# Kernel tuning notes

Measured on AMD Instinct MI355X. Metric: run time of the kernel, lower is better.

## Reference

```python
import jax, jax.numpy as jnp
import numpy as np

EMBED_DIM = 768
NUM_HEADS = 12


def setup_inputs() -> dict:
    key = jax.random.key(0)
    ks = jax.random.split(key, 9)
    C = EMBED_DIM
    x = jax.random.normal(ks[0], (8, 3136, C), dtype=jnp.float32)
    s = 0.02
    Wq = jax.random.normal(ks[1], (C, C), dtype=jnp.float32) * s
    Wk = jax.random.normal(ks[2], (C, C), dtype=jnp.float32) * s
    Wv = jax.random.normal(ks[3], (C, C), dtype=jnp.float32) * s
    Wo = jax.random.normal(ks[4], (C, C), dtype=jnp.float32) * s
    bq = jax.random.normal(ks[5], (C,), dtype=jnp.float32) * s
    bk = jax.random.normal(ks[6], (C,), dtype=jnp.float32) * s
    bv = jax.random.normal(ks[7], (C,), dtype=jnp.float32) * s
    bo = jax.random.normal(ks[8], (C,), dtype=jnp.float32) * s
    return {"x": x, "Wq": Wq, "bq": bq, "Wk": Wk, "bk": bk,
            "Wv": Wv, "bv": bv, "Wo": Wo, "bo": bo, "T": 16}


def reference(x, Wq, bq, Wk, bk, Wv, bv, Wo, bo, T):
    B, N, C = x.shape
    H = NUM_HEADS
    hd = C // H
    Hh = H // 2
    P = N // T
    scale = 1.0 / np.sqrt(hd).astype(np.float32)

    Q = (x @ Wq + bq).reshape(B, T, P, H, hd)
    K = (x @ Wk + bk).reshape(B, T, P, H, hd)
    V = (x @ Wv + bv).reshape(B, T, P, H, hd)

    # spatial attention: first Hh heads, attend over patches within each frame
    Qs, Ks, Vs = Q[..., :Hh, :], K[..., :Hh, :], V[..., :Hh, :]
    scores_s = jnp.einsum('btphd,btqhd->bthpq', Qs, Ks) * scale  # (B,T,Hh,P,P)
    ws = jax.nn.softmax(scores_s, axis=-1)
    out_s = jnp.einsum('bthpq,btqhd->btphd', ws, Vs)  # (B,T,P,Hh,hd)

    # temporal attention: last Hh heads, attend over frames at each patch
    Qt, Kt, Vt = Q[..., Hh:, :], K[..., Hh:, :], V[..., Hh:, :]
    scores_t = jnp.einsum('btphd,bsphd->bphts', Qt, Kt) * scale  # (B,P,Hh,T,T)
    wt = jax.nn.softmax(scores_t, axis=-1)
    out_t = jnp.einsum('bphts,bsphd->btphd', wt, Vt)  # (B,T,P,Hh,hd)

    out = jnp.concatenate([out_s, out_t], axis=3).reshape(B, N, C)
    return out @ Wo + bo
```

## Files before the change

### kernel.cpp

```cpp
#include <hip/hip_runtime.h>


typedef __attribute__((ext_vector_type(8))) short short8;
typedef __attribute__((ext_vector_type(4))) float f32x4;

typedef __attribute__((address_space(1))) void gvoid;
typedef __attribute__((address_space(3))) void lvoid;

__device__ __forceinline__ unsigned short f2b(float f) {
  unsigned int u = __float_as_uint(f);
  unsigned int r = (u + 0x7FFFu + ((u >> 16) & 1u)) >> 16;
  return (unsigned short)r;
}

__global__ __launch_bounds__(256) void k_convert_x(
    const float* __restrict__ x, unsigned short* __restrict__ xb,
    const float* __restrict__ bq, const float* __restrict__ bk,
    const float* __restrict__ bv, float* __restrict__ bqkv) {
  int tid = blockIdx.x * 256 + threadIdx.x;
  if (tid < 2304)
    bqkv[tid] = tid < 768 ? bq[tid] : (tid < 1536 ? bk[tid - 768] : bv[tid - 1536]);
  float4 v = ((const float4*)x)[tid];
  ushort4 o;
  o.x = f2b(v.x); o.y = f2b(v.y); o.z = f2b(v.z); o.w = f2b(v.w);
  ((ushort4*)xb)[tid] = o;
}

__global__ __launch_bounds__(256) void k_pack_w(
    const float* __restrict__ Wq, const float* __restrict__ Wk,
    const float* __restrict__ Wv, const float* __restrict__ Wo,
    unsigned short* __restrict__ wqkvT, unsigned short* __restrict__ woT) {
  __shared__ float tile[32][33];
  int bid = blockIdx.x;
  const float* W;
  unsigned short* dst;
  int n0, k0;
  if (bid < 1728) {
    int tn = bid % 72, tk = bid / 72;
    n0 = tn * 32; k0 = tk * 32;
    int which = n0 / 768;
    W = which == 0 ? Wq : (which == 1 ? Wk : Wv);
    dst = wqkvT;
  } else {
    int b2 = bid - 1728;
    int tn = b2 % 24, tk = b2 / 24;
    n0 = tn * 32; k0 = tk * 32;
    W = Wo; dst = woT;
  }
  int nn0 = n0 % 768;
  for (int i = threadIdx.x; i < 1024; i += 256) {
    int r = i >> 5, c = i & 31;
    tile[r][c] = W[(size_t)(k0 + r) * 768 + nn0 + c];
  }
  __syncthreads();
  for (int i = threadIdx.x; i < 1024; i += 256) {
    int r = i >> 5, c = i & 31;
    dst[(size_t)(n0 + r) * 768 + k0 + c] = f2b(tile[c][r]);
  }
}

template <int OUTF32>
__global__ __launch_bounds__(256) void k_gemm_bt(
    const unsigned short* __restrict__ A, const unsigned short* __restrict__ Bt,
    const float* __restrict__ bias, void* __restrict__ Cout,
    int M, int N, int K) {
  __shared__ __align__(16) unsigned short As[128 * 32];
  __shared__ __align__(16) unsigned short Bs[128 * 32];
  const int tid = threadIdx.x;
  const int w = tid >> 6, l = tid & 63;
  const int lg = l >> 4, ln = l & 15;
  const int m0 = blockIdx.y * 128, n0 = blockIdx.x * 128;
  const int wr = (w >> 1) * 64, wc = (w & 1) * 64;
  f32x4 acc[4][4] = {};
  const unsigned short* ga = A + (size_t)(m0 + (tid >> 2)) * K + ((tid & 3) * 8);
  const unsigned short* gb = Bt + (size_t)(n0 + (tid >> 2)) * K + ((tid & 3) * 8);
  unsigned short* lAs = As + w * 512;
  unsigned short* lBs = Bs + w * 512;
  const size_t krow64 = (size_t)64 * K;
  for (int k0 = 0; k0 < K; k0 += 32) {
    __builtin_amdgcn_global_load_lds((const gvoid*)(ga + k0),          (lvoid*)lAs,          16, 0, 0);
    __builtin_amdgcn_global_load_lds((const gvoid*)(ga + krow64 + k0), (lvoid*)(lAs + 2048), 16, 0, 0);
    __builtin_amdgcn_global_load_lds((const gvoid*)(gb + k0),          (lvoid*)lBs,          16, 0, 0);
    __builtin_amdgcn_global_load_lds((const gvoid*)(gb + krow64 + k0), (lvoid*)(lBs + 2048), 16, 0, 0);
    __syncthreads();
    short8 a[4], b[4];
#pragma unroll
    for (int mt = 0; mt < 4; ++mt)
      a[mt] = *(const short8*)(As + (wr + mt * 16 + ln) * 32 + lg * 8);
#pragma unroll
    for (int nt = 0; nt < 4; ++nt)
      b[nt] = *(const short8*)(Bs + (wc + nt * 16 + ln) * 32 + lg * 8);
#pragma unroll
    for (int mt = 0; mt < 4; ++mt)
#pragma unroll
      for (int nt = 0; nt < 4; ++nt)
        acc[mt][nt] = __builtin_amdgcn_mfma_f32_16x16x32_bf16(a[mt], b[nt], acc[mt][nt], 0, 0, 0);
    __syncthreads();
  }
#pragma unroll
  for (int nt = 0; nt < 4; ++nt) {
    int col = n0 + wc + nt * 16 + ln;
    float bval = bias[col];
#pragma unroll
    for (int mt = 0; mt < 4; ++mt) {
      int row = m0 + wr + mt * 16 + lg * 4;
#pragma unroll
      for (int r = 0; r < 4; ++r) {
        float v = acc[mt][nt][r] + bval;
        if (OUTF32)
          ((float*)Cout)[(size_t)(row + r) * N + col] = v;
        else
          ((unsigned short*)Cout)[(size_t)(row + r) * N + col] = f2b(v);
      }
    }
  }
}

__global__ __launch_bounds__(256) void k_attn_spatial(
    const unsigned short* __restrict__ qkv, unsigned short* __restrict__ attn) {
  const int bi = blockIdx.x;
  const int h = bi % 6;
  const int t = (bi / 6) % 16;
  const int b = bi / 96;
  const int base_row = b * 3136 + t * 196;
  __shared__ __align__(16) unsigned short Vt[64][232];
  __shared__ __align__(16) unsigned short Pl[4][16][232];
  for (int i = threadIdx.x; i < 196 * 64; i += 256) {
    int key = i >> 6, d = i & 63;
    Vt[d][key] = qkv[(size_t)(base_row + key) * 2304 + 1536 + h * 64 + d];
  }
  for (int i = threadIdx.x; i < 64 * 28; i += 256)
    Vt[i / 28][196 + (i % 28)] = 0;
  __syncthreads();
  const int w = threadIdx.x >> 6, l = threadIdx.x & 63;
  const int lg = l >> 4, ln = l & 15;
  const float scale = 0.125f;
  for (int mt = w; mt < 13; mt += 4) {
    int qm = mt * 16 + ln; if (qm > 195) qm = 195;
    const size_t qoff = (size_t)(base_row + qm) * 2304 + h * 64 + lg * 8;
    short8 qa0 = *(const short8*)(qkv + qoff);
    short8 qa1 = *(const short8*)(qkv + qoff + 32);
    f32x4 st[13];
#pragma unroll
    for (int nt = 0; nt < 13; ++nt) {
      int kn = nt * 16 + ln; if (kn > 195) kn = 195;
      const size_t koff = (size_t)(base_row + kn) * 2304 + 768 + h * 64 + lg * 8;
      short8 kb0 = *(const short8*)(qkv + koff);
      short8 kb1 = *(const short8*)(qkv + koff + 32);
      f32x4 s = {0.f, 0.f, 0.f, 0.f};
      s = __builtin_amdgcn_mfma_f32_16x16x32_bf16(qa0, kb0, s, 0, 0, 0);
      s = __builtin_amdgcn_mfma_f32_16x16x32_bf16(qa1, kb1, s, 0, 0, 0);
      st[nt] = s;
    }
    float mr[4] = {-1e30f, -1e30f, -1e30f, -1e30f};
#pragma unroll
    for (int nt = 0; nt < 13; ++nt) {
      bool valid = (nt * 16 + ln) < 196;
#pragma unroll
      for (int r = 0; r < 4; ++r) {
        float v = valid ? st[nt][r] * scale : -1e30f;
        st[nt][r] = v;
        mr[r] = fmaxf(mr[r], v);
      }
    }
#pragma unroll
    for (int msk = 1; msk <= 8; msk <<= 1)
#pragma unroll
      for (int r = 0; r < 4; ++r) mr[r] = fmaxf(mr[r], __shfl_xor(mr[r], msk));
    float sm[4] = {0.f, 0.f, 0.f, 0.f};
#pragma unroll
    for (int nt = 0; nt < 13; ++nt)
#pragma unroll
      for (int r = 0; r < 4; ++r) {
        float p = __expf(st[nt][r] - mr[r]);
        st[nt][r] = p;
        sm[r] += p;
      }
#pragma unroll
    for (int msk = 1; msk <= 8; msk <<= 1)
#pragma unroll
      for (int r = 0; r < 4; ++r) sm[r] += __shfl_xor(sm[r], msk);
    float inv[4];
#pragma unroll
    for (int r = 0; r < 4; ++r) inv[r] = 1.f / sm[r];
#pragma unroll
    for (int nt = 0; nt < 13; ++nt)
#pragma unroll
      for (int r = 0; r < 4; ++r)
        Pl[w][lg * 4 + r][nt * 16 + ln] = f2b(st[nt][r] * inv[r]);
#pragma unroll
    for (int r = 0; r < 4; ++r) Pl[w][ln][208 + lg * 4 + r] = 0;
#pragma unroll
    for (int nt4 = 0; nt4 < 4; ++nt4) {
      f32x4 acc = {0.f, 0.f, 0.f, 0.f};
#pragma unroll
      for (int ks = 0; ks < 7; ++ks) {
        short8 pa = *(const short8*)(&Pl[w][ln][ks * 32 + lg * 8]);
        short8 vb = *(const short8*)(&Vt[nt4 * 16 + ln][ks * 32 + lg * 8]);
        acc = __builtin_amdgcn_mfma_f32_16x16x32_bf16(pa, vb, acc, 0, 0, 0);
      }
#pragma unroll
      for (int r = 0; r < 4; ++r) {
        int m = mt * 16 + lg * 4 + r;
        if (m < 196)
          attn[(size_t)(base_row + m) * 768 + h * 64 + nt4 * 16 + ln] = f2b(acc[r]);
      }
    }
  }
}

__global__ __launch_bounds__(256) void k_attn_temporal(
    const unsigned short* __restrict__ qkv, unsigned short* __restrict__ attn) {
  const int w = threadIdx.x >> 6, l = threadIdx.x & 63;
  const int u = blockIdx.x * 4 + w;
  const int b = u / 1176;
  const int rem = u % 1176;
  const int p = rem / 6;
  const int h = 6 + rem % 6;
  const size_t rowb = (size_t)b * 3136 + p;
  __shared__ __align__(16) unsigned short Vt[4][64][40];
  __shared__ __align__(16) unsigned short Pl[4][16][40];
  for (int i = l; i < 1024; i += 64) {
    int tt = i >> 6, d = i & 63;
    Vt[w][d][tt] = qkv[(rowb + (size_t)tt * 196) * 2304 + 1536 + h * 64 + d];
  }
  for (int i = l; i < 1024; i += 64)
    Vt[w][i >> 4][16 + (i & 15)] = 0;
  const int lg = l >> 4, ln = l & 15;
  const size_t qoff = (rowb + (size_t)ln * 196) * 2304 + h * 64 + lg * 8;
  short8 qa0 = *(const short8*)(qkv + qoff);
  short8 qa1 = *(const short8*)(qkv + qoff + 32);
  short8 kb0 = *(const short8*)(qkv + qoff + 768);
  short8 kb1 = *(const short8*)(qkv + qoff + 768 + 32);
  f32x4 s = {0.f, 0.f, 0.f, 0.f};
  s = __builtin_amdgcn_mfma_f32_16x16x32_bf16(qa0, kb0, s, 0, 0, 0);
  s = __builtin_amdgcn_mfma_f32_16x16x32_bf16(qa1, kb1, s, 0, 0, 0);
  const float scale = 0.125f;
  float stv[4], mr[4];
#pragma unroll
  for (int r = 0; r < 4; ++r) { stv[r] = s[r] * scale; mr[r] = stv[r]; }
#pragma unroll
  for (int msk = 1; msk <= 8; msk <<= 1)
#pragma unroll
    for (int r = 0; r < 4; ++r) mr[r] = fmaxf(mr[r], __shfl_xor(mr[r], msk));
  float sm[4];
#pragma unroll
  for (int r = 0; r < 4; ++r) { stv[r] = __expf(stv[r] - mr[r]); sm[r] = stv[r]; }
#pragma unroll
  for (int msk = 1; msk <= 8; msk <<= 1)
#pragma unroll
    for (int r = 0; r < 4; ++r) sm[r] += __shfl_xor(sm[r], msk);
#pragma unroll
  for (int r = 0; r < 4; ++r)
    Pl[w][lg * 4 + r][ln] = f2b(stv[r] / sm[r]);
#pragma unroll
  for (int r = 0; r < 4; ++r) Pl[w][ln][16 + lg * 4 + r] = 0;
  short8 pa = *(const short8*)(&Pl[w][ln][lg * 8]);
#pragma unroll
  for (int nt4 = 0; nt4 < 4; ++nt4) {
    short8 vb = *(const short8*)(&Vt[w][nt4 * 16 + ln][lg * 8]);
    f32x4 acc = {0.f, 0.f, 0.f, 0.f};
    acc = __builtin_amdgcn_mfma_f32_16x16x32_bf16(pa, vb, acc, 0, 0, 0);
#pragma unroll
    for (int r = 0; r < 4; ++r) {
      int tq = lg * 4 + r;
      attn[((size_t)b * 3136 + (size_t)tq * 196 + p) * 768 + h * 64 + nt4 * 16 + ln] = f2b(acc[r]);
    }
  }
}

extern "C" void kernel_launch(void* const* d_in, const int* in_sizes, int n_in,
                              void* d_out, int out_size, void* d_ws, size_t ws_size,
                              hipStream_t stream) {
  const float* x  = (const float*)d_in[0];
  const float* Wq = (const float*)d_in[1];
  const float* bq = (const float*)d_in[2];
  const float* Wk = (const float*)d_in[3];
  const float* bk = (const float*)d_in[4];
  const float* Wv = (const float*)d_in[5];
  const float* bv = (const float*)d_in[6];
  const float* Wo = (const float*)d_in[7];
  const float* bo = (const float*)d_in[8];
  float* out = (float*)d_out;
  char* ws = (char*)d_ws;
  unsigned short* xb    = (unsigned short*)(ws + 0);
  unsigned short* wqkvT = (unsigned short*)(ws + 38535168);
  float*          bqkv  = (float*)(ws + 42074112);
  unsigned short* woT   = (unsigned short*)(ws + 42083328);
  unsigned short* qkvb  = (unsigned short*)(ws + 43262976);
  unsigned short* attnb = (unsigned short*)(ws + 158868480);

  k_convert_x<<<18816, 256, 0, stream>>>(x, xb, bq, bk, bv, bqkv);
  k_pack_w<<<2304, 256, 0, stream>>>(Wq, Wk, Wv, Wo, wqkvT, woT);
  k_gemm_bt<0><<<dim3(18, 196), 256, 0, stream>>>(xb, wqkvT, bqkv, (void*)qkvb, 25088, 2304, 768);
  k_attn_spatial<<<768, 256, 0, stream>>>(qkvb, attnb);
  k_attn_temporal<<<2352, 256, 0, stream>>>(qkvb, attnb);
  k_gemm_bt<1><<<dim3(6, 196), 256, 0, stream>>>(attnb, woT, bo, (void*)out, 25088, 768, 768);
}
```

Measured before the change: 282.5 us.

## Replace QKV projection GEMM with 256x256 tiled, LDS-direct pipelined bf16 kernel

Adds a new QKV projection GEMM that uses 256x256 output tiles with 8 waves, loads global memory straight into LDS with global_load_lds, and double-buffers the K dimension. The loads are interleaved with MFMA phases and paired with a swizzled LDS layout and an XCD-aware remapping of workgroups. The goal is more data reuse per tile, less LDS bank conflict, and better overlap of memory and compute than the old 128x128 kernel. In exchange the hand-scheduled waitcnt and barrier choreography is complex and fragile, and the kernel is hardcoded to K=768.

```diff
diff --git a/kernel.cpp b/kernel.cpp
--- a/kernel.cpp
+++ b/kernel.cpp
@@ -57,6 +57,143 @@
     int r = i >> 5, c = i & 31;
     dst[(size_t)(n0 + r) * 768 + k0 + c] = f2b(tile[c][r]);
   }
+}
+
+
+#define FENCE asm volatile("" ::: "memory")
+#define BARRIER do { FENCE; __builtin_amdgcn_s_barrier(); FENCE; } while (0)
+#define WAIT_LGKM0 asm volatile("s_waitcnt lgkmcnt(0)" ::: "memory")
+#define WAIT_VM4 asm volatile("s_waitcnt vmcnt(4)" ::: "memory")
+
+#define STAGE(PBASE, BUFBASE, HT, KT_) do {                                          \
+    int kt__ = (KT_);                                                                \
+    bool real__ = (kt__ < 12);                                                       \
+    if (!real__) kt__ -= 12;                                                         \
+    const unsigned short* src__ = (PBASE) + (HT) * 98304 + kt__ * 64;                \
+    unsigned d0__ = real__ ? ((BUFBASE) + (HT) * 8192 + w * 512) : (65536u + w * 512); \
+    unsigned d1__ = real__ ? ((BUFBASE) + (HT) * 8192 + 4096 + w * 512) : (65536u + w * 512); \
+    __builtin_amdgcn_global_load_lds((const gvoid*)src__, (lvoid*)(lds + d0__), 16, 0, 0); \
+    __builtin_amdgcn_global_load_lds((const gvoid*)(src__ + 49152), (lvoid*)(lds + d1__), 16, 0, 0); \
+  } while (0)
+
+#define LDA(MH, ABASE) do {                                                          \
+    const unsigned short* ab__ = lds + (ABASE) + ((MH) * 128 + arow) * 64;           \
+    _Pragma("unroll")                                                                \
+    for (int mf = 0; mf < 4; ++mf) {                                                 \
+      af[mf][0] = *(const short8*)(ab__ + mf * 1024 + s0);                           \
+      af[mf][1] = *(const short8*)(ab__ + mf * 1024 + s1);                           \
+    }                                                                                \
+  } while (0)
+
+#define LDB(NH, BBASE) do {                                                          \
+    const unsigned short* bb__ = lds + (BBASE) + ((NH) * 128 + brow) * 64;           \
+    _Pragma("unroll")                                                                \
+    for (int nf = 0; nf < 2; ++nf) {                                                 \
+      bf[nf][0] = *(const short8*)(bb__ + nf * 1024 + s0);                           \
+      bf[nf][1] = *(const short8*)(bb__ + nf * 1024 + s1);                           \
+    }                                                                                \
+  } while (0)
+
+#define MM(MH, NH) do {                                                              \
+    __builtin_amdgcn_s_setprio(1);                                                   \
+    _Pragma("unroll")                                                                \
+    for (int mf = 0; mf < 4; ++mf) {                                                 \
+      _Pragma("unroll")                                                              \
+      for (int nf = 0; nf < 2; ++nf) {                                               \
+        acc[MH][mf][NH][nf] = __builtin_amdgcn_mfma_f32_16x16x32_bf16(               \
+            af[mf][0], bf[nf][0], acc[MH][mf][NH][nf], 0, 0, 0);                     \
+        acc[MH][mf][NH][nf] = __builtin_amdgcn_mfma_f32_16x16x32_bf16(               \
+            af[mf][1], bf[nf][1], acc[MH][mf][NH][nf], 0, 0, 0);                     \
+      }                                                                              \
+    }                                                                                \
+    __builtin_amdgcn_s_setprio(0);                                                   \
+  } while (0)
+
+__global__ __launch_bounds__(512, 2) void k_gemm256(
+    const unsigned short* __restrict__ A, const unsigned short* __restrict__ Bt,
+    const float* __restrict__ bias, unsigned short* __restrict__ Cout,
+    int M, int N) {
+  __shared__ __align__(16) unsigned short lds[69632];
+  const int nwg = gridDim.x;
+  const int nbx = N >> 8;
+  const int orig = blockIdx.x;
+  const int q = nwg >> 3, r = nwg & 7;
+  const int xcd = orig & 7, lin = orig >> 3;
+  const int wg = (xcd < r ? xcd * (q + 1) : r * (q + 1) + (xcd - r) * q) + lin;
+  const int m0 = (wg / nbx) << 8, n0 = (wg % nbx) << 8;
+
+  const int tid = threadIdx.x;
+  const int w = tid >> 6, l = tid & 63;
+  const int wm = w >> 2, wn = w & 3;
+  const int lg = l >> 4, ln = l & 15;
+  const int arow = wm * 64 + ln;
+  const int brow = wn * 32 + ln;
+  const int s0 = (lg ^ (ln & 7)) * 8;
+  const int s1 = s0 ^ 32;
+  const int srow = tid >> 3;
+  const int slg8 = ((tid & 7) ^ (srow & 7)) * 8;
+  const unsigned short* pA = A + (size_t)(m0 + srow) * 768 + slg8;
+  const unsigned short* pB = Bt + (size_t)(n0 + srow) * 768 + slg8;
+
+  f32x4 acc[2][4][2][2] = {};
+
+  STAGE(pA, 0,     0, 0);
+  STAGE(pB, 16384, 1, 0);
+  STAGE(pA, 0,     1, 0);
+  STAGE(pB, 16384, 0, 0);
+  STAGE(pA, 32768, 0, 1);
+  STAGE(pB, 49152, 1, 1);
+  STAGE(pA, 32768, 1, 1);
+  asm volatile("s_waitcnt vmcnt(6)" ::: "memory");
+  __builtin_amdgcn_s_barrier();
+  FENCE;
+
+  for (int it = 0; it < 6; ++it) {
+    const int kt1 = 2 * it + 1, ktn0 = 2 * it + 2, ktn1 = 2 * it + 3;
+    short8 af[4][2], bf[2][2];
+    LDA(0, 0); LDB(0, 16384);
+    STAGE(pB, 49152, 0, kt1);
+    BARRIER; WAIT_LGKM0; MM(0, 0); BARRIER;
+    LDB(1, 16384);
+    STAGE(pA, 0, 0, ktn0);
+    BARRIER; WAIT_LGKM0; MM(0, 1); BARRIER;
+    LDA(1, 0);
+    STAGE(pB, 16384, 1, ktn0);
+    BARRIER; WAIT_LGKM0; MM(1, 1); BARRIER;
+    LDB(0, 16384);
+    STAGE(pA, 0, 1, ktn0);
+    WAIT_VM4;
+    BARRIER; WAIT_LGKM0; MM(1, 0); BARRIER;
+    LDA(0, 32768); LDB(0, 49152);
+    STAGE(pB, 16384, 0, ktn0);
+    BARRIER; WAIT_LGKM0; MM(0, 0); BARRIER;
+    LDB(1, 49152);
+    STAGE(pA, 32768, 0, ktn1);
+    BARRIER; WAIT_LGKM0; MM(0, 1); BARRIER;
+    LDA(1, 32768);
+    STAGE(pB, 49152, 1, ktn1);
+    BARRIER; WAIT_LGKM0; MM(1, 1); BARRIER;
+    LDB(0, 49152);
+    STAGE(pA, 32768, 1, ktn1);
+    WAIT_VM4;
+    BARRIER; WAIT_LGKM0; MM(1, 0); BARRIER;
+  }
+
+#pragma unroll
+  for (int mh = 0; mh < 2; ++mh)
+#pragma unroll
+    for (int mf = 0; mf < 4; ++mf)
+#pragma unroll
+      for (int nh = 0; nh < 2; ++nh)
+#pragma unroll
+        for (int nf = 0; nf < 2; ++nf) {
+          const int col = n0 + nh * 128 + wn * 32 + nf * 16 + ln;
+          const float bval = bias[col];
+          const int row = m0 + mh * 128 + wm * 64 + mf * 16 + lg * 4;
+#pragma unroll
+          for (int rr = 0; rr < 4; ++rr)
+            Cout[(size_t)(row + rr) * N + col] = f2b(acc[mh][mf][nh][nf][rr] + bval);
+        }
 }
 
 template <int OUTF32>
@@ -292,7 +429,7 @@
 
   k_convert_x<<<18816, 256, 0, stream>>>(x, xb, bq, bk, bv, bqkv);
   k_pack_w<<<2304, 256, 0, stream>>>(Wq, Wk, Wv, Wo, wqkvT, woT);
-  k_gemm_bt<0><<<dim3(18, 196), 256, 0, stream>>>(xb, wqkvT, bqkv, (void*)qkvb, 25088, 2304, 768);
+  k_gemm256<<<882, 512, 0, stream>>>(xb, wqkvT, bqkv, qkvb, 25088, 2304);
   k_attn_spatial<<<768, 256, 0, stream>>>(qkvb, attnb);
   k_attn_temporal<<<2352, 256, 0, stream>>>(qkvb, attnb);
   k_gemm_bt<1><<<dim3(6, 196), 256, 0, stream>>>(attnb, woT, bo, (void*)out, 25088, 768, 768);
```

Measured after the change: 257.5 us. 1.1x faster.
